# Kernel optimization log

Measured on AMD Instinct MI355X. Metric: run time of the kernel, lower is better.

## Reference

```python
import jax, jax.numpy as jnp
import numpy as np

EPS = 1e-09
TOP_K = 2


def setup_inputs() -> dict:
    key = jax.random.key(0)
    k1, k2 = jax.random.split(key)
    N, D, E = 32768, 1024, 64
    x = jax.random.normal(k1, (N, D), dtype=jnp.float32)
    gate_w = jax.random.normal(k2, (E, D), dtype=jnp.float32) * (1.0 / np.sqrt(D))
    return {"x": x, "gate_w": gate_w}


def reference(x, gate_w):
    # logits: [N, E] = x @ gate_w.T  (nn.Linear with no bias)
    logits = jnp.einsum("nd,ed->ne", x, gate_w)
    probs = jax.nn.softmax(logits, axis=-1)
    # aux load-balancing loss (stored on buffer in torch; returned here)
    mean_probs = probs.mean(axis=0)  # [E]
    aux_loss = jnp.sum(mean_probs * jnp.log(mean_probs + EPS))
    # top-k selection + renormalize
    top_k_weights, top_k_indices = jax.lax.top_k(probs, TOP_K)  # [N, K]
    top_k_weights = top_k_weights / (top_k_weights.sum(axis=-1, keepdims=True) + EPS)
    return top_k_weights, top_k_indices, aux_loss
```

## Files before the change

### kernel.cpp

```cpp
#include <hip/hip_runtime.h>
#include <hip/hip_bf16.h>
#include <math.h>

#define NROWS 32768
#define DDIM  1024
#define NEXP  64
#define TAU   2e-4f
#define EPSF  1e-9f
#define CAPMAX 8192
#define NSHARD 8
#define NCH   32

typedef __attribute__((ext_vector_type(8)))  short  short8;
typedef __attribute__((ext_vector_type(16))) float  f32x16;
typedef __attribute__((address_space(3))) unsigned int       lds_u32;
typedef __attribute__((address_space(1))) const unsigned int g_u32;

__device__ __forceinline__ bool gt_(float a, int ea, float b, int eb)
{ return a > b || (a == b && ea < eb); }

__device__ __forceinline__ void cvt_hl(float f, short& h, short& l)
{
    __hip_bfloat16 hb = __float2bfloat16(f);
    float r = f - __bfloat162float(hb);
    __hip_bfloat16 lb = __float2bfloat16(r);
    h = *reinterpret_cast<short*>(&hb);
    l = *reinterpret_cast<short*>(&lb);
}

__global__ void wpack_kernel(const float* __restrict__ gw,
                             unsigned short* __restrict__ wp,
                             float* __restrict__ shard,
                             int* __restrict__ cnt)
{
    if (blockIdx.x == 0) {
        shard[threadIdx.x]       = 0.0f;
        shard[256 + threadIdx.x] = 0.0f;
        if (threadIdx.x == 0) *cnt = 0;
    }
    const int kc = blockIdx.x;
    const int t  = threadIdx.x;
    const int lane = t & 63, g = (t >> 6) & 1, pr = t >> 7;
    const int e = g * 32 + (lane & 31);
    const int k = kc * 16 + (lane >> 5) * 8;
    float4 f0 = *reinterpret_cast<const float4*>(gw + (size_t)e * DDIM + k);
    float4 f1 = *reinterpret_cast<const float4*>(gw + (size_t)e * DDIM + k + 4);
    float f[8] = {f0.x, f0.y, f0.z, f0.w, f1.x, f1.y, f1.z, f1.w};
    short8 o;
    #pragma unroll
    for (int j = 0; j < 8; ++j) {
        short hh, ll;
        cvt_hl(f[j], hh, ll);
        o[j] = pr ? ll : hh;
    }
    *reinterpret_cast<short8*>(wp + ((size_t)((kc * 2 + g) * 2 + pr) * 64 + lane) * 8) = o;
}

__global__ __launch_bounds__(256, 2) void moe_main(
    const float* __restrict__ x, const unsigned short* __restrict__ wp,
    float* __restrict__ out, float* __restrict__ shard,
    int* __restrict__ cnt, int* __restrict__ list, int cap)
{
    extern __shared__ char smem[];

    const int t = threadIdx.x;
    const int wave = t >> 6, lane = t & 63;
    const int wm = wave & 1, g = wave >> 1;
    const int l31 = lane & 31, l5 = lane >> 5;
    const int row0 = blockIdx.x * 64;
    const int arow = wm * 32 + l31;
    const int xr   = (arow & 7) << 4;

    f32x16 acc;
    #pragma unroll
    for (int r = 0; r < 16; ++r) acc[r] = 0.0f;

    int srow[2], scol[2];
    #pragma unroll
    for (int q = 0; q < 2; ++q) {
        int d = q * 4096 + t * 16;
        srow[q] = d >> 7;
        scol[q] = (d & 127) ^ ((srow[q] & 7) << 4);
    }

    #define STAGE(c_) do {                                                       \
        const char* xs0_ = (const char*)x + (size_t)row0 * 4096 + (size_t)(c_) * 128; \
        const char* bs0_ = (const char*)wp + (size_t)(c_) * 8192;                \
        const int xb_ = ((c_) & 3) * 8192;                                       \
        const int bb_ = 32768 + ((c_) & 3) * 8192;                               \
        _Pragma("unroll")                                                        \
        for (int q_ = 0; q_ < 2; ++q_) {                                         \
            int d_ = q_ * 4096 + t * 16;                                         \
            const char* xsrc_ = xs0_ + (size_t)srow[q_] * 4096 + scol[q_];       \
            __builtin_amdgcn_global_load_lds((g_u32*)xsrc_,                      \
                (lds_u32*)(smem + xb_ + d_), 16, 0, 0);                          \
            __builtin_amdgcn_global_load_lds((g_u32*)(bs0_ + d_),                \
                (lds_u32*)(smem + bb_ + d_), 16, 0, 0);                          \
        }                                                                        \
    } while (0)

    STAGE(0); STAGE(1); STAGE(2);

    for (int i = 0; i < NCH; ++i) {
        if (i < NCH - 3) {
            STAGE(i + 3);
            __builtin_amdgcn_sched_barrier(0);
            asm volatile("s_waitcnt vmcnt(12)" ::: "memory");
        } else if (i == NCH - 3) {
            asm volatile("s_waitcnt vmcnt(8)" ::: "memory");
        } else if (i == NCH - 2) {
            asm volatile("s_waitcnt vmcnt(4)" ::: "memory");
        } else {
            asm volatile("s_waitcnt vmcnt(0)" ::: "memory");
        }
        __builtin_amdgcn_s_barrier();
        __builtin_amdgcn_sched_barrier(0);

        const int xb = (i & 3) * 8192;
        const int bb = 32768 + (i & 3) * 8192;
        #pragma unroll
        for (int kcl = 0; kcl < 2; ++kcl) {
            const int cb = kcl * 64 + l5 * 32;
            const char* xrow = smem + xb + arow * 128;
            float4 f0 = *reinterpret_cast<const float4*>(xrow + (cb ^ xr));
            float4 f1 = *reinterpret_cast<const float4*>(xrow + ((cb + 16) ^ xr));
            float f[8] = {f0.x, f0.y, f0.z, f0.w, f1.x, f1.y, f1.z, f1.w};
            short8 ah, al;
            #pragma unroll
            for (int jj = 0; jj < 8; ++jj) {
                short hh, ll;
                cvt_hl(f[jj], hh, ll);
                ah[jj] = hh; al[jj] = ll;
            }
            const char* bp = smem + bb + ((kcl * 2 + g) * 2) * 1024 + lane * 16;
            short8 bh = *reinterpret_cast<const short8*>(bp);
            short8 bl = *reinterpret_cast<const short8*>(bp + 1024);
            acc = __builtin_amdgcn_mfma_f32_32x32x16_bf16(ah, bh, acc, 0, 0, 0);
            acc = __builtin_amdgcn_mfma_f32_32x32x16_bf16(al, bh, acc, 0, 0, 0);
            acc = __builtin_amdgcn_mfma_f32_32x32x16_bf16(ah, bl, acc, 0, 0, 0);
        }
        __builtin_amdgcn_sched_barrier(0);
        __builtin_amdgcn_s_barrier();
        __builtin_amdgcn_sched_barrier(0);
    }
    #undef STAGE

    float* lgs = reinterpret_cast<float*>(smem);
    __syncthreads();
    #pragma unroll
    for (int r = 0; r < 16; ++r) {
        const int lrow = wm * 32 + (r & 3) + 8 * (r >> 2) + 4 * l5;
        lgs[lrow * 68 + g * 32 + l31] = acc[r];
    }
    __syncthreads();

    const int erow = t >> 2, q = t & 3;
    float L[16];
    #pragma unroll
    for (int i = 0; i < 4; ++i) {
        float4 v = *reinterpret_cast<const float4*>(lgs + erow * 68 + q * 16 + i * 4);
        L[4*i] = v.x; L[4*i+1] = v.y; L[4*i+2] = v.z; L[4*i+3] = v.w;
    }
    float v1 = -3.4e38f, v2 = -3.4e38f, v3 = -3.4e38f;
    int   e1 = 1 << 30,  e2 = 1 << 30,  e3 = 1 << 30;
    #pragma unroll
    for (int i = 0; i < 16; ++i) {
        float v = L[i]; int e = q * 16 + i;
        if      (gt_(v, e, v1, e1)) { v3=v2; e3=e2; v2=v1; e2=e1; v1=v; e1=e; }
        else if (gt_(v, e, v2, e2)) { v3=v2; e3=e2; v2=v; e2=e; }
        else if (gt_(v, e, v3, e3)) { v3=v; e3=e; }
    }
    #pragma unroll
    for (int m = 1; m <= 2; m <<= 1) {
        float o1 = __shfl_xor(v1, m), o2 = __shfl_xor(v2, m), o3 = __shfl_xor(v3, m);
        int  oe1 = __shfl_xor(e1, m), oe2 = __shfl_xor(e2, m), oe3 = __shfl_xor(e3, m);
        float n1, n2, n3; int m1, m2, m3;
        if (gt_(v1, e1, o1, oe1)) {
            n1 = v1; m1 = e1;
            if (gt_(v2, e2, o1, oe1)) {
                n2 = v2; m2 = e2;
                if (gt_(v3, e3, o1, oe1)) { n3 = v3; m3 = e3; } else { n3 = o1; m3 = oe1; }
            } else {
                n2 = o1; m2 = oe1;
                if (gt_(v2, e2, o2, oe2)) { n3 = v2; m3 = e2; } else { n3 = o2; m3 = oe2; }
            }
        } else {
            n1 = o1; m1 = oe1;
            if (gt_(o2, oe2, v1, e1)) {
                n2 = o2; m2 = oe2;
                if (gt_(o3, oe3, v1, e1)) { n3 = o3; m3 = oe3; } else { n3 = v1; m3 = e1; }
            } else {
                n2 = v1; m2 = e1;
                if (gt_(o2, oe2, v2, e2)) { n3 = o2; m3 = oe2; } else { n3 = v2; m3 = e2; }
            }
        }
        v1 = n1; e1 = m1; v2 = n2; e2 = m2; v3 = n3; e3 = m3;
    }
    float pr[16], sl = 0.0f;
    #pragma unroll
    for (int i = 0; i < 16; ++i) { pr[i] = expf(L[i] - v1); sl += pr[i]; }
    float S = sl;
    S += __shfl_xor(S, 1); S += __shfl_xor(S, 2);
    const float invS = 1.0f / S;
    #pragma unroll
    for (int i = 0; i < 16; ++i) pr[i] *= invS;
    #pragma unroll
    for (int m = 4; m <= 32; m <<= 1)
        #pragma unroll
        for (int i = 0; i < 16; ++i) pr[i] += __shfl_xor(pr[i], m);
    float* auxred = lgs + 64 * 68;
    if (lane < 4) {
        #pragma unroll
        for (int i = 0; i < 16; ++i) auxred[wave * 64 + q * 16 + i] = pr[i];
    }
    if (q == 0) {
        const float p1 = invS;
        const float p2 = expf(v2 - v1) * invS;
        const float dn = p1 + p2 + EPSF;
        const int r = row0 + erow;
        out[2 * r]                 = p1 / dn;
        out[2 * r + 1]             = p2 / dn;
        out[2 * NROWS + 2 * r]     = (float)e1;
        out[2 * NROWS + 2 * r + 1] = (float)e2;
        if (cap > 0 && (v1 - v2 < TAU || v2 - v3 < TAU)) {
            int pos = atomicAdd(cnt, 1);
            if (pos < cap) list[pos] = r;
        }
    }
    __syncthreads();
    if (t < 64) {
        float s = auxred[t] + auxred[64 + t] + auxred[128 + t] + auxred[192 + t];
        atomicAdd(&shard[(blockIdx.x & (NSHARD - 1)) * 64 + t], s);
    }
}

__global__ __launch_bounds__(256) void finalize_kernel(
    const float* __restrict__ x, const float* __restrict__ gw,
    float* __restrict__ out, const float* __restrict__ shard,
    const int* __restrict__ cnt, const int* __restrict__ list, int cap)
{
    if (blockIdx.x == 0) {
        const int tt = threadIdx.x;
        if (tt < 64) {
            float m = 0.0f;
            #pragma unroll
            for (int s = 0; s < NSHARD; ++s) m += shard[s * 64 + tt];
            m *= (1.0f / (float)NROWS);
            float v = m * logf(m + EPSF);
            #pragma unroll
            for (int k = 1; k <= 32; k <<= 1) v += __shfl_xor(v, k);
            if (tt == 0) out[4 * NROWS] = v;
        }
        return;
    }
    __shared__ float lg[64];
    const int n = (cap > 0) ? min(*cnt, cap) : 0;
    const int tt = threadIdx.x, e = tt >> 2, part = tt & 3;
    for (int j = (int)blockIdx.x - 1; j < n; j += 64) {
        const int row = list[j];
        const float* xrp = x  + (size_t)row * DDIM + part * 256;
        const float* wrp = gw + (size_t)e   * DDIM + part * 256;
        float a = 0.0f;
        #pragma unroll 8
        for (int kk = 0; kk < 64; ++kk) {
            float4 xv = *reinterpret_cast<const float4*>(xrp + kk * 4);
            float4 wv = *reinterpret_cast<const float4*>(wrp + kk * 4);
            a += xv.x * wv.x + xv.y * wv.y + xv.z * wv.z + xv.w * wv.w;
        }
        a += __shfl_xor(a, 1); a += __shfl_xor(a, 2);
        if (part == 0) lg[e] = a;
        __syncthreads();
        if (tt < 4) {
            const int q = tt;
            float v1 = -3.4e38f, v2 = -3.4e38f; int e1 = 1 << 30, e2 = 1 << 30;
            float Lr[16];
            #pragma unroll
            for (int i = 0; i < 16; ++i) {
                float v = Lr[i] = lg[q * 16 + i]; int ee = q * 16 + i;
                if      (gt_(v, ee, v1, e1)) { v2 = v1; e2 = e1; v1 = v; e1 = ee; }
                else if (gt_(v, ee, v2, e2)) { v2 = v; e2 = ee; }
            }
            #pragma unroll
            for (int m = 1; m <= 2; m <<= 1) {
                float o1 = __shfl_xor(v1, m), o2 = __shfl_xor(v2, m);
                int  oe1 = __shfl_xor(e1, m), oe2 = __shfl_xor(e2, m);
                float n1, n2; int m1, m2;
                if (gt_(v1, e1, o1, oe1)) {
                    n1 = v1; m1 = e1;
                    if (gt_(v2, e2, o1, oe1)) { n2 = v2; m2 = e2; } else { n2 = o1; m2 = oe1; }
                } else {
                    n1 = o1; m1 = oe1;
                    if (gt_(o2, oe2, v1, e1)) { n2 = o2; m2 = oe2; } else { n2 = v1; m2 = e1; }
                }
                v1 = n1; e1 = m1; v2 = n2; e2 = m2;
            }
            float s = 0.0f;
            #pragma unroll
            for (int i = 0; i < 16; ++i) s += expf(Lr[i] - v1);
            s += __shfl_xor(s, 1); s += __shfl_xor(s, 2);
            if (q == 0) {
                const float invS = 1.0f / s;
                const float p1 = invS, p2 = expf(v2 - v1) * invS;
                const float dn = p1 + p2 + EPSF;
                out[2 * row]                 = p1 / dn;
                out[2 * row + 1]             = p2 / dn;
                out[2 * NROWS + 2 * row]     = (float)e1;
                out[2 * NROWS + 2 * row + 1] = (float)e2;
            }
        }
        __syncthreads();
    }
}

extern "C" void kernel_launch(void* const* d_in, const int* in_sizes, int n_in,
                              void* d_out, int out_size, void* d_ws, size_t ws_size,
                              hipStream_t stream)
{
    const float* x  = (const float*)d_in[0];
    const float* gw = (const float*)d_in[1];
    float* out      = (float*)d_out;

    unsigned short* wp = (unsigned short*)d_ws;
    float* shard   = (float*)((char*)d_ws + 262144);
    int*   cnt     = (int*)((char*)d_ws + 264192);
    int*   list    = (int*)((char*)d_ws + 264448);
    int cap = 0;
    if (ws_size >= 264448 + 4096) {
        size_t avail = (ws_size - 264448) / sizeof(int);
        cap = (avail > CAPMAX) ? CAPMAX : (int)avail;
    }

    hipLaunchKernelGGL(wpack_kernel, dim3(64), dim3(256), 0, stream,
                       gw, wp, shard, cnt);
    hipLaunchKernelGGL(moe_main, dim3(NROWS / 64), dim3(256), 65536, stream,
                       x, wp, out, shard, cnt, list, cap);
    hipLaunchKernelGGL(finalize_kernel, dim3(65), dim3(256), 0, stream,
                       x, gw, out, shard, cnt, list, cap);
}
```

Measured before the change: 61.03 us.

## Load packed gate weights directly to registers, halve LDS and raise occupancy

Packed bf16 gate-weight fragments are now loaded straight from global memory into registers, one chunk ahead, instead of being staged through LDS. LDS use per block drops from 64KB to 32KB and launch bounds move to 4 blocks per CU, so more waves can hide memory latency. The vmcnt waits are retuned to match the new mix of loads. The costs are more VGPR pressure, which may cap occupancy or cause spills, and the weight fragments being re-read from L2 by each wave.

```diff
diff --git a/kernel.cpp b/kernel.cpp
--- a/kernel.cpp
+++ b/kernel.cpp
@@ -56,7 +56,7 @@
     *reinterpret_cast<short8*>(wp + ((size_t)((kc * 2 + g) * 2 + pr) * 64 + lane) * 8) = o;
 }
 
-__global__ __launch_bounds__(256, 2) void moe_main(
+__global__ __launch_bounds__(256, 4) void moe_main(
     const float* __restrict__ x, const unsigned short* __restrict__ wp,
     float* __restrict__ out, float* __restrict__ shard,
     int* __restrict__ cnt, int* __restrict__ list, int cap)
@@ -83,41 +83,46 @@
         scol[q] = (d & 127) ^ ((srow[q] & 7) << 4);
     }
 
+    const char* wqb = (const char*)wp + (size_t)g * 2048 + (size_t)lane * 16;
+
     #define STAGE(c_) do {                                                       \
         const char* xs0_ = (const char*)x + (size_t)row0 * 4096 + (size_t)(c_) * 128; \
-        const char* bs0_ = (const char*)wp + (size_t)(c_) * 8192;                \
         const int xb_ = ((c_) & 3) * 8192;                                       \
-        const int bb_ = 32768 + ((c_) & 3) * 8192;                               \
         _Pragma("unroll")                                                        \
         for (int q_ = 0; q_ < 2; ++q_) {                                         \
             int d_ = q_ * 4096 + t * 16;                                         \
             const char* xsrc_ = xs0_ + (size_t)srow[q_] * 4096 + scol[q_];       \
             __builtin_amdgcn_global_load_lds((g_u32*)xsrc_,                      \
                 (lds_u32*)(smem + xb_ + d_), 16, 0, 0);                          \
-            __builtin_amdgcn_global_load_lds((g_u32*)(bs0_ + d_),                \
-                (lds_u32*)(smem + bb_ + d_), 16, 0, 0);                          \
         }                                                                        \
     } while (0)
 
+    #define BLOAD(dst0, dst1, dst2, dst3, c_) do {                               \
+        const char* b_ = wqb + (size_t)(c_) * 8192;                              \
+        dst0 = *reinterpret_cast<const short8*>(b_);                             \
+        dst1 = *reinterpret_cast<const short8*>(b_ + 1024);                      \
+        dst2 = *reinterpret_cast<const short8*>(b_ + 4096);                      \
+        dst3 = *reinterpret_cast<const short8*>(b_ + 5120);                      \
+    } while (0)
+
+    short8 Bc0, Bc1, Bc2, Bc3, Bn0, Bn1, Bn2, Bn3;
+
     STAGE(0); STAGE(1); STAGE(2);
+    BLOAD(Bc0, Bc1, Bc2, Bc3, 0);
 
     for (int i = 0; i < NCH; ++i) {
-        if (i < NCH - 3) {
-            STAGE(i + 3);
-            __builtin_amdgcn_sched_barrier(0);
-            asm volatile("s_waitcnt vmcnt(12)" ::: "memory");
-        } else if (i == NCH - 3) {
-            asm volatile("s_waitcnt vmcnt(8)" ::: "memory");
-        } else if (i == NCH - 2) {
-            asm volatile("s_waitcnt vmcnt(4)" ::: "memory");
-        } else {
-            asm volatile("s_waitcnt vmcnt(0)" ::: "memory");
-        }
+        if (i < NCH - 1) BLOAD(Bn0, Bn1, Bn2, Bn3, i + 1);
+        if (i < NCH - 3) STAGE(i + 3);
+        __builtin_amdgcn_sched_barrier(0);
+        if (i == 0)               { asm volatile("s_waitcnt vmcnt(6)" ::: "memory"); }
+        else if (i < NCH - 3)     { asm volatile("s_waitcnt vmcnt(8)" ::: "memory"); }
+        else if (i == NCH - 3)    { asm volatile("s_waitcnt vmcnt(6)" ::: "memory"); }
+        else if (i == NCH - 2)    { asm volatile("s_waitcnt vmcnt(4)" ::: "memory"); }
+        else                      { asm volatile("s_waitcnt vmcnt(0)" ::: "memory"); }
         __builtin_amdgcn_s_barrier();
         __builtin_amdgcn_sched_barrier(0);
 
         const int xb = (i & 3) * 8192;
-        const int bb = 32768 + (i & 3) * 8192;
         #pragma unroll
         for (int kcl = 0; kcl < 2; ++kcl) {
             const int cb = kcl * 64 + l5 * 32;
@@ -132,18 +137,19 @@
                 cvt_hl(f[jj], hh, ll);
                 ah[jj] = hh; al[jj] = ll;
             }
-            const char* bp = smem + bb + ((kcl * 2 + g) * 2) * 1024 + lane * 16;
-            short8 bh = *reinterpret_cast<const short8*>(bp);
-            short8 bl = *reinterpret_cast<const short8*>(bp + 1024);
+            short8 bh = kcl ? Bc2 : Bc0;
+            short8 bl = kcl ? Bc3 : Bc1;
             acc = __builtin_amdgcn_mfma_f32_32x32x16_bf16(ah, bh, acc, 0, 0, 0);
             acc = __builtin_amdgcn_mfma_f32_32x32x16_bf16(al, bh, acc, 0, 0, 0);
             acc = __builtin_amdgcn_mfma_f32_32x32x16_bf16(ah, bl, acc, 0, 0, 0);
         }
+        Bc0 = Bn0; Bc1 = Bn1; Bc2 = Bn2; Bc3 = Bn3;
         __builtin_amdgcn_sched_barrier(0);
         __builtin_amdgcn_s_barrier();
         __builtin_amdgcn_sched_barrier(0);
     }
     #undef STAGE
+    #undef BLOAD
 
     float* lgs = reinterpret_cast<float*>(smem);
     __syncthreads();
@@ -332,7 +338,7 @@
 
     hipLaunchKernelGGL(wpack_kernel, dim3(64), dim3(256), 0, stream,
                        gw, wp, shard, cnt);
-    hipLaunchKernelGGL(moe_main, dim3(NROWS / 64), dim3(256), 65536, stream,
+    hipLaunchKernelGGL(moe_main, dim3(NROWS / 64), dim3(256), 32768, stream,
                        x, wp, out, shard, cnt, list, cap);
     hipLaunchKernelGGL(finalize_kernel, dim3(65), dim3(256), 0, stream,
                        x, gw, out, shard, cnt, list, cap);
```

Result: no change. 61.65 us (+1.0%).
